# Kernel optimization log

Measured on AMD Instinct MI355X. Metric: run time of the kernel, lower is better.

The kernel has to match this reference:

```python
import jax, jax.numpy as jnp
import numpy as np

EMBED = 1024
HEADS = 16
HEAD_DIM = EMBED // HEADS
SEQ = 2048
BATCH = 2


def setup_inputs() -> dict:
    key = jax.random.key(0)
    ks = jax.random.split(key, 5)
    s = 1.0 / np.sqrt(EMBED)
    return {
        "x": jax.random.normal(ks[0], (BATCH, SEQ, EMBED), jnp.float32),
        "W_qkv": jax.random.uniform(ks[1], (EMBED, 3 * EMBED), jnp.float32, -s, s),
        "b_qkv": jax.random.uniform(ks[2], (3 * EMBED,), jnp.float32, -s, s),
        "W_out": jax.random.uniform(ks[3], (EMBED, EMBED), jnp.float32, -s, s),
        "b_out": jax.random.uniform(ks[4], (EMBED,), jnp.float32, -s, s),
    }


def reference(x, W_qkv, b_qkv, W_out, b_out):
    B, S, E = x.shape
    qkv = x @ W_qkv + b_qkv                      # [B,S,3E]
    q, k, v = jnp.split(qkv, 3, axis=-1)
    # [B,S,E] -> [B,H,S,D]
    def heads(t):
        return t.reshape(B, S, HEADS, HEAD_DIM).transpose(0, 2, 1, 3)
    q, k, v = heads(q), heads(k), heads(v)
    scores = jnp.einsum("bhid,bhjd->bhij", q, k) / np.sqrt(HEAD_DIM)  # [B,H,S,S]
    causal = jnp.tril(jnp.ones((S, S), bool))
    scores = jnp.where(causal[None, None], scores, -jnp.inf)
    probs = jax.nn.softmax(scores, axis=-1)
    out = jnp.einsum("bhij,bhjd->bhid", probs, v)  # [B,H,S,D]
    out = out.transpose(0, 2, 1, 3).reshape(B, S, E)
    return out @ W_out + b_out
```

## Files before the change

kernel.cpp:

```cpp
#include <hip/hip_runtime.h>
#include <hip/hip_bf16.h>
#include <cstdint>
#include <cstddef>


typedef unsigned short u16;
typedef __attribute__((ext_vector_type(8))) short short8;
typedef __attribute__((ext_vector_type(4))) short short4v;
typedef __attribute__((ext_vector_type(4))) float floatx4;

#define MFMA16(a, b, c) __builtin_amdgcn_mfma_f32_16x16x32_bf16((a), (b), (c), 0, 0, 0)

#if __has_builtin(__builtin_amdgcn_mfma_f32_16x16x16_bf16)
#define PV_MFMA(a, b, c) __builtin_amdgcn_mfma_f32_16x16x16_bf16((a), (b), (c), 0, 0, 0)
#elif __has_builtin(__builtin_amdgcn_mfma_f32_16x16x16bf16_1k)
#define PV_MFMA(a, b, c) __builtin_amdgcn_mfma_f32_16x16x16bf16_1k((a), (b), (c), 0, 0, 0)
#else
static __device__ __forceinline__ floatx4 pv_mfma_asm(short4v a, short4v b, floatx4 c) {
    asm volatile("v_mfma_f32_16x16x16_bf16 %0, %1, %2, %0" : "+v"(c) : "v"(a), "v"(b));
    return c;
}
#define PV_MFMA(a, b, c) pv_mfma_asm((a), (b), (c))
#endif

#if __has_builtin(__builtin_amdgcn_exp2f)
#define EXP2(x) __builtin_amdgcn_exp2f(x)
#else
#define EXP2(x) exp2f(x)
#endif

#define QSCALE 0.18033688011f

static __device__ __forceinline__ u16 f2b(float f) {
    union { float f; uint32_t u; } v; v.f = f;
    return (u16)((v.u + 0x7fffu + ((v.u >> 16) & 1u)) >> 16);
}

static __device__ __forceinline__ uint32_t pkbf(float lo, float hi) {
    union { float f; uint32_t u; } a, b; a.f = lo; b.f = hi;
    return __builtin_amdgcn_perm(b.u + 0x8000u, a.u + 0x8000u, 0x07060302u);
}

static __device__ __forceinline__ void async_cp16(const u16* g, u16* lds_wave_base) {
    __builtin_amdgcn_global_load_lds((__attribute__((address_space(1))) void*)g,
                                     (__attribute__((address_space(3))) void*)lds_wave_base,
                                     16, 0, 0);
}


__global__ __launch_bounds__(256) void k_f32_to_bf16(const float* __restrict__ src,
                                                     u16* __restrict__ dst, int n8) {
    int g = blockIdx.x * 256 + threadIdx.x;
    if (g >= n8) return;
    const float4* s = (const float4*)src + (size_t)g * 2;
    float4 f0 = s[0];
    float4 f1 = s[1];
    alignas(16) u16 r[8] = {f2b(f0.x), f2b(f0.y), f2b(f0.z), f2b(f0.w),
                            f2b(f1.x), f2b(f1.y), f2b(f1.z), f2b(f1.w)};
    *(uint4*)(dst + (size_t)g * 8) = *(const uint4*)r;
}

__global__ __launch_bounds__(256) void k_transpose_to_bf16(const float* __restrict__ src,
                                                           u16* __restrict__ dst,
                                                           int R, int C) {
    __shared__ float t[32][33];
    int tx = threadIdx.x, ty = threadIdx.y;
    int c0 = blockIdx.x * 32, r0 = blockIdx.y * 32;
#pragma unroll
    for (int i = 0; i < 4; ++i)
        t[ty + i * 8][tx] = src[(size_t)(r0 + ty + i * 8) * C + c0 + tx];
    __syncthreads();
#pragma unroll
    for (int i = 0; i < 4; ++i)
        dst[(size_t)(c0 + ty + i * 8) * R + r0 + tx] = f2b(t[tx][ty + i * 8]);
}


__global__ __launch_bounds__(256) void k_qkv_gemm(const u16* __restrict__ A,
                                                  const u16* __restrict__ Bt,
                                                  const float* __restrict__ bias,
                                                  u16* __restrict__ Qb,
                                                  u16* __restrict__ Kb,
                                                  u16* __restrict__ Vtb) {
    __shared__ __align__(16) u16 As[128 * 64];
    __shared__ __align__(16) u16 Bs[128 * 64];
    int tid = threadIdx.x;
    int w = tid >> 6, lane = tid & 63, quad = lane >> 4, l16 = lane & 15;
    int wm = w >> 1, wn = w & 1;
    int m0 = blockIdx.y * 128, n0 = blockIdx.x * 128;
    int wb8 = (tid & ~63) * 8;
    floatx4 acc[4][4] = {};

    for (int kt = 0; kt < 16; ++kt) {
#pragma unroll
        for (int i = 0; i < 4; ++i) {
            int f = i * 256 + tid;
            int r = f >> 3, c = (f & 7) ^ (r & 7);
            async_cp16(&A[(size_t)(m0 + r) * 1024 + kt * 64 + c * 8], &As[i * 2048 + wb8]);
        }
#pragma unroll
        for (int i = 0; i < 4; ++i) {
            int f = i * 256 + tid;
            int r = f >> 3, c = (f & 7) ^ (r & 7);
            async_cp16(&Bt[(size_t)(n0 + r) * 1024 + kt * 64 + c * 8], &Bs[i * 2048 + wb8]);
        }
        __syncthreads();
#pragma unroll
        for (int ks = 0; ks < 2; ++ks) {
            short8 af[4], bf[4];
            int sw = l16 & 7;
#pragma unroll
            for (int mt = 0; mt < 4; ++mt)
                af[mt] = *(const short8*)&As[((wm * 64 + mt * 16 + l16) * 8 + ((ks * 4 + quad) ^ sw)) * 8];
#pragma unroll
            for (int nt = 0; nt < 4; ++nt)
                bf[nt] = *(const short8*)&Bs[((wn * 64 + nt * 16 + l16) * 8 + ((ks * 4 + quad) ^ sw)) * 8];
#pragma unroll
            for (int mt = 0; mt < 4; ++mt)
#pragma unroll
                for (int nt = 0; nt < 4; ++nt)
                    acc[mt][nt] = MFMA16(af[mt], bf[nt], acc[mt][nt]);
        }
        __syncthreads();
    }

    int region = n0 >> 10;
    if (region == 2) {
#pragma unroll
        for (int mt = 0; mt < 4; ++mt)
#pragma unroll
            for (int nt = 0; nt < 4; ++nt) {
                int n_abs = n0 + wn * 64 + nt * 16 + l16;
                int e = n_abs & 1023, h = e >> 6, d = e & 63;
                float vb = bias[n_abs];
                int mrow = m0 + wm * 64 + mt * 16 + quad * 4;
                int b = mrow >> 11, s0 = mrow & 2047;
                uint2 val;
                val.x = pkbf(acc[mt][nt][0] + vb, acc[mt][nt][1] + vb);
                val.y = pkbf(acc[mt][nt][2] + vb, acc[mt][nt][3] + vb);
                *(uint2*)&Vtb[((size_t)(b * 16 + h) * 64 + d) * 2048 + s0] = val;
            }
    } else {
        u16* dst = region == 0 ? Qb : Kb;
        float scl = region == 0 ? QSCALE : 1.0f;
#pragma unroll
        for (int mt = 0; mt < 4; ++mt)
#pragma unroll
            for (int nt = 0; nt < 4; ++nt)
#pragma unroll
                for (int r = 0; r < 4; ++r) {
                    int m_abs = m0 + wm * 64 + mt * 16 + quad * 4 + r;
                    int n_abs = n0 + wn * 64 + nt * 16 + l16;
                    float val = (acc[mt][nt][r] + bias[n_abs]) * scl;
                    int e = n_abs & 1023, h = e >> 6, d = e & 63;
                    int b = m_abs >> 11, s = m_abs & 2047;
                    dst[((size_t)(b * 16 + h) * 2048 + s) * 64 + d] = f2b(val);
                }
    }
}


__global__ __launch_bounds__(256) void k_out_gemm(const u16* __restrict__ A,
                                                  const u16* __restrict__ Bt,
                                                  const float* __restrict__ bias,
                                                  float* __restrict__ out) {
    __shared__ __align__(16) u16 As[64 * 64];
    __shared__ __align__(16) u16 Bs[128 * 64];
    int tid = threadIdx.x;
    int w = tid >> 6, lane = tid & 63, quad = lane >> 4, l16 = lane & 15;
    int wm = w >> 1, wn = w & 1;
    int m0 = blockIdx.y * 64, n0 = blockIdx.x * 128;
    int wb8 = (tid & ~63) * 8;
    floatx4 acc[2][4] = {};

    for (int kt = 0; kt < 16; ++kt) {
#pragma unroll
        for (int i = 0; i < 2; ++i) {
            int f = i * 256 + tid;
            int r = f >> 3, c = (f & 7) ^ (r & 7);
            async_cp16(&A[(size_t)(m0 + r) * 1024 + kt * 64 + c * 8], &As[i * 2048 + wb8]);
        }
#pragma unroll
        for (int i = 0; i < 4; ++i) {
            int f = i * 256 + tid;
            int r = f >> 3, c = (f & 7) ^ (r & 7);
            async_cp16(&Bt[(size_t)(n0 + r) * 1024 + kt * 64 + c * 8], &Bs[i * 2048 + wb8]);
        }
        __syncthreads();
#pragma unroll
        for (int ks = 0; ks < 2; ++ks) {
            short8 af[2], bf[4];
            int sw = l16 & 7;
#pragma unroll
            for (int mt = 0; mt < 2; ++mt)
                af[mt] = *(const short8*)&As[((wm * 32 + mt * 16 + l16) * 8 + ((ks * 4 + quad) ^ sw)) * 8];
#pragma unroll
            for (int nt = 0; nt < 4; ++nt)
                bf[nt] = *(const short8*)&Bs[((wn * 64 + nt * 16 + l16) * 8 + ((ks * 4 + quad) ^ sw)) * 8];
#pragma unroll
            for (int mt = 0; mt < 2; ++mt)
#pragma unroll
                for (int nt = 0; nt < 4; ++nt)
                    acc[mt][nt] = MFMA16(af[mt], bf[nt], acc[mt][nt]);
        }
        __syncthreads();
    }

#pragma unroll
    for (int mt = 0; mt < 2; ++mt)
#pragma unroll
        for (int nt = 0; nt < 4; ++nt)
#pragma unroll
            for (int r = 0; r < 4; ++r) {
                int m_abs = m0 + wm * 32 + mt * 16 + quad * 4 + r;
                int n_abs = n0 + wn * 64 + nt * 16 + l16;
                out[(size_t)m_abs * 1024 + n_abs] = acc[mt][nt][r] + bias[n_abs];
            }
}


__global__ __launch_bounds__(256, 2) void k_attn(const u16* __restrict__ Qb,
                                                 const u16* __restrict__ Kb,
                                                 const u16* __restrict__ Vtb,
                                                 u16* __restrict__ attnb) {
    __shared__ __align__(16) u16 KV[4][2][4096];
    int tid = threadIdx.x;
    int w = tid >> 6, lane = tid & 63, quad = lane >> 4, l16 = lane & 15;
    int L = blockIdx.x;
    int bh = ((L & 7) << 2) | ((L >> 3) & 3);
    int pr = L >> 5;
    int qta = pr, qtb = 31 - pr;
    const u16* Qp = Qb + (size_t)bh * 131072;
    const u16* Kp = Kb + (size_t)bh * 131072;
    const u16* Vp = Vtb + (size_t)bh * 131072;

    int r0 = tid >> 3, c0 = ((tid & 7) ^ (r0 & 7)) * 8;
    int f1 = 256 + tid;
    int r1 = f1 >> 3, c1 = ((f1 & 7) ^ (r1 & 7)) * 8;
    int kOff0 = r0 * 64 + c0, kOff1 = r1 * 64 + c1;
    int vOff0 = r0 * 2048 + c0, vOff1 = r1 * 2048 + c1;
    int wb = (tid & ~63) * 8;

    int qrowa = qta * 64 + w * 16 + l16;
    int qrowb = qtb * 64 + w * 16 + l16;
    short8 qa0 = *(const short8*)&Qp[(size_t)qrowa * 64 + quad * 8];
    short8 qa1 = *(const short8*)&Qp[(size_t)qrowa * 64 + 32 + quad * 8];
    short8 qb0 = *(const short8*)&Qp[(size_t)qrowb * 64 + quad * 8];
    short8 qb1 = *(const short8*)&Qp[(size_t)qrowb * 64 + 32 + quad * 8];

    int na = qta + 1;
    int n = na + qtb + 1;

    auto stage = [&](int j) {
        int kt = (j < na) ? j : (j - na);
        u16* Ks = (u16*)KV[j & 3][0];
        u16* Vs = (u16*)KV[j & 3][1];
        const u16* kp = Kp + (size_t)kt * 4096;
        const u16* vp = Vp + (size_t)kt * 64;
        async_cp16(kp + kOff0, Ks + wb);
        async_cp16(kp + kOff1, Ks + 2048 + wb);
        async_cp16(vp + vOff0, Vs + wb);
        async_cp16(vp + vOff1, Vs + 2048 + wb);
    };

    floatx4 accO[4] = {};
    float m_run = -__builtin_inff(), l_run = 0.f;
    int sw = l16 & 7;
    int kt = 0, qt = qta, q0 = qta * 64;
    short8 cq0 = qa0, cq1 = qa1;
    int b = bh >> 4, h = bh & 15;

    stage(0); stage(1); stage(2);

    for (int j = 0; j < n; ++j) {
        asm volatile("s_waitcnt vmcnt(8)" ::: "memory");
        asm volatile("s_barrier" ::: "memory");
        {
            int jn = j + 3;
            stage(jn < n ? jn : n - 1);
        }
        const u16* Ks = (const u16*)KV[j & 3][0];
        const u16* Vs = (const u16*)KV[j & 3][1];

        floatx4 sa[4] = {};
#pragma unroll
        for (int nt = 0; nt < 4; ++nt) {
            int rb = (nt * 16 + l16) * 8;
            short8 kfa = *(const short8*)&Ks[(rb + (quad ^ sw)) * 8];
            short8 kfb = *(const short8*)&Ks[(rb + ((4 + quad) ^ sw)) * 8];
            sa[nt] = MFMA16(kfa, cq0, sa[nt]);
            sa[nt] = MFMA16(kfb, cq1, sa[nt]);
        }
        if (kt == qt) {
            int q_abs = q0 + w * 16 + l16;
#pragma unroll
            for (int nt = 0; nt < 4; ++nt)
#pragma unroll
                for (int r = 0; r < 4; ++r)
                    if (kt * 64 + nt * 16 + quad * 4 + r > q_abs)
                        sa[nt][r] = -__builtin_inff();
        }
        float v = sa[0][0];
#pragma unroll
        for (int nt = 0; nt < 4; ++nt)
#pragma unroll
            for (int r = 0; r < 4; ++r) v = fmaxf(v, sa[nt][r]);
        v = fmaxf(v, __shfl_xor(v, 16));
        v = fmaxf(v, __shfl_xor(v, 32));
        float m_new = fmaxf(m_run, v);
        float alpha = EXP2(m_run - m_new);
        float p[4][4];
        float rs = 0.f;
#pragma unroll
        for (int nt = 0; nt < 4; ++nt)
#pragma unroll
            for (int r = 0; r < 4; ++r) {
                float e = EXP2(sa[nt][r] - m_new);
                p[nt][r] = e;
                rs += e;
            }
        rs += __shfl_xor(rs, 16);
        rs += __shfl_xor(rs, 32);
        l_run = l_run * alpha + rs;
        m_run = m_new;
        float al[4];
#pragma unroll
        for (int r = 0; r < 4; ++r) al[r] = __shfl(alpha, quad * 4 + r, 16);
#pragma unroll
        for (int dt = 0; dt < 4; ++dt)
#pragma unroll
            for (int r = 0; r < 4; ++r) accO[dt][r] *= al[r];
#pragma unroll
        for (int nt = 0; nt < 4; ++nt) {
            union { uint2 u; short4v s; } pf;
            pf.u.x = pkbf(p[nt][0], p[nt][1]);
            pf.u.y = pkbf(p[nt][2], p[nt][3]);
#pragma unroll
            for (int dt = 0; dt < 4; ++dt) {
                int row = dt * 16 + l16;
                int chunk = nt * 2 + (quad >> 1);
                const char* vb2 = (const char*)Vs + row * 128 + ((chunk ^ (row & 7)) * 16) + (quad & 1) * 8;
                short4v vf = *(const short4v*)vb2;
                accO[dt] = PV_MFMA(pf.s, vf, accO[dt]);
            }
        }

        if (kt == qt) {
            float lbc[4];
#pragma unroll
            for (int r = 0; r < 4; ++r) lbc[r] = __shfl(l_run, quad * 4 + r, 16);
#pragma unroll
            for (int r = 0; r < 4; ++r) {
                float inv = 1.f / lbc[r];
                int q_abs = q0 + w * 16 + quad * 4 + r;
                size_t base = ((size_t)(b * 2048 + q_abs)) * 1024 + h * 64;
#pragma unroll
                for (int dt = 0; dt < 4; ++dt)
                    attnb[base + dt * 16 + l16] = f2b(accO[dt][r] * inv);
            }
#pragma unroll
            for (int dt = 0; dt < 4; ++dt) accO[dt] = floatx4{0.f, 0.f, 0.f, 0.f};
            m_run = -__builtin_inff();
            l_run = 0.f;
            kt = 0;
            qt = qtb;
            q0 = qtb * 64;
            cq0 = qb0;
            cq1 = qb1;
        } else {
            ++kt;
        }
    }
}


extern "C" void kernel_launch(void* const* d_in, const int* in_sizes, int n_in,
                              void* d_out, int out_size, void* d_ws, size_t ws_size,
                              hipStream_t stream) {
    const float* x     = (const float*)d_in[0];
    const float* W_qkv = (const float*)d_in[1];
    const float* b_qkv = (const float*)d_in[2];
    const float* W_out = (const float*)d_in[3];
    const float* b_out = (const float*)d_in[4];
    float* out = (float*)d_out;

    char* p = (char*)d_ws;
    u16* xb    = (u16*)p; p += (size_t)4096 * 1024 * 2;
    u16* wqkvT = (u16*)p; p += (size_t)3072 * 1024 * 2;
    u16* woutT = (u16*)p; p += (size_t)1024 * 1024 * 2;
    u16* Qb    = (u16*)p; p += (size_t)32 * 2048 * 64 * 2;
    u16* Kb    = (u16*)p; p += (size_t)32 * 2048 * 64 * 2;
    u16* Vtb   = (u16*)p; p += (size_t)32 * 64 * 2048 * 2;
    u16* attnb = xb;

    k_f32_to_bf16<<<(4096 * 1024 / 8) / 256, 256, 0, stream>>>(x, xb, 4096 * 1024 / 8);
    dim3 tb(32, 8);
    k_transpose_to_bf16<<<dim3(3072 / 32, 1024 / 32), tb, 0, stream>>>(W_qkv, wqkvT, 1024, 3072);
    k_transpose_to_bf16<<<dim3(1024 / 32, 1024 / 32), tb, 0, stream>>>(W_out, woutT, 1024, 1024);
    k_qkv_gemm<<<dim3(24, 32), 256, 0, stream>>>(xb, wqkvT, b_qkv, Qb, Kb, Vtb);
    k_attn<<<512, 256, 0, stream>>>(Qb, Kb, Vtb, attnb);
    k_out_gemm<<<dim3(8, 64), 256, 0, stream>>>(attnb, woutT, b_out, out);
}
```

Baseline: 194.1 us.

## Share K/V tiles between both paired query tiles in causal attention loop

Instead of streaming K/V separately for the short and long query tiles in sequence, the loop now walks only the long tile's key range and applies each loaded K/V tile to both query tiles, computing the short tile only while kt <= qta. This halves K/V staging and LDS fragment reads for the overlapping range. The PV MFMA operands are swapped so the output is transposed, which lets the epilogue write packed bf16 vectors without cross-lane alpha/l broadcasts. Block-to-tile pairing is also remapped to spread heavy and light tiles differently. The cost is higher register pressure from two accumulators and the preloaded V fragments.

```diff
diff --git a/kernel.cpp b/kernel.cpp
--- a/kernel.cpp
+++ b/kernel.cpp
@@ -228,11 +228,13 @@
     int w = tid >> 6, lane = tid & 63, quad = lane >> 4, l16 = lane & 15;
     int L = blockIdx.x;
     int bh = ((L & 7) << 2) | ((L >> 3) & 3);
-    int pr = L >> 5;
+    int idx = (L >> 5) & 15;
+    int pr = idx < 8 ? idx : 23 - idx;
     int qta = pr, qtb = 31 - pr;
     const u16* Qp = Qb + (size_t)bh * 131072;
     const u16* Kp = Kb + (size_t)bh * 131072;
     const u16* Vp = Vtb + (size_t)bh * 131072;
+    int b = bh >> 4, h = bh & 15;
 
     int r0 = tid >> 3, c0 = ((tid & 7) ^ (r0 & 7)) * 8;
     int f1 = 256 + tid;
@@ -248,129 +250,127 @@
     short8 qb0 = *(const short8*)&Qp[(size_t)qrowb * 64 + quad * 8];
     short8 qb1 = *(const short8*)&Qp[(size_t)qrowb * 64 + 32 + quad * 8];
 
-    int na = qta + 1;
-    int n = na + qtb + 1;
+    int n = qtb + 1;
 
     auto stage = [&](int j) {
-        int kt = (j < na) ? j : (j - na);
         u16* Ks = (u16*)KV[j & 3][0];
         u16* Vs = (u16*)KV[j & 3][1];
-        const u16* kp = Kp + (size_t)kt * 4096;
-        const u16* vp = Vp + (size_t)kt * 64;
+        const u16* kp = Kp + (size_t)j * 4096;
+        const u16* vp = Vp + (size_t)j * 64;
         async_cp16(kp + kOff0, Ks + wb);
         async_cp16(kp + kOff1, Ks + 2048 + wb);
         async_cp16(vp + vOff0, Vs + wb);
         async_cp16(vp + vOff1, Vs + 2048 + wb);
     };
 
-    floatx4 accO[4] = {};
-    float m_run = -__builtin_inff(), l_run = 0.f;
+    floatx4 accA[4] = {}, accB[4] = {};
+    float ma = -__builtin_inff(), la = 0.f;
+    float mb = -__builtin_inff(), lb = 0.f;
     int sw = l16 & 7;
-    int kt = 0, qt = qta, q0 = qta * 64;
-    short8 cq0 = qa0, cq1 = qa1;
-    int b = bh >> 4, h = bh & 15;
 
     stage(0); stage(1); stage(2);
 
-    for (int j = 0; j < n; ++j) {
+    for (int kt = 0; kt < n; ++kt) {
         asm volatile("s_waitcnt vmcnt(8)" ::: "memory");
         asm volatile("s_barrier" ::: "memory");
         {
-            int jn = j + 3;
+            int jn = kt + 3;
             stage(jn < n ? jn : n - 1);
         }
-        const u16* Ks = (const u16*)KV[j & 3][0];
-        const u16* Vs = (const u16*)KV[j & 3][1];
-
-        floatx4 sa[4] = {};
+        const u16* Ks = (const u16*)KV[kt & 3][0];
+        const u16* Vs = (const u16*)KV[kt & 3][1];
+
+        short8 kfa[4], kfb[4];
 #pragma unroll
         for (int nt = 0; nt < 4; ++nt) {
             int rb = (nt * 16 + l16) * 8;
-            short8 kfa = *(const short8*)&Ks[(rb + (quad ^ sw)) * 8];
-            short8 kfb = *(const short8*)&Ks[(rb + ((4 + quad) ^ sw)) * 8];
-            sa[nt] = MFMA16(kfa, cq0, sa[nt]);
-            sa[nt] = MFMA16(kfb, cq1, sa[nt]);
-        }
-        if (kt == qt) {
-            int q_abs = q0 + w * 16 + l16;
+            kfa[nt] = *(const short8*)&Ks[(rb + (quad ^ sw)) * 8];
+            kfb[nt] = *(const short8*)&Ks[(rb + ((4 + quad) ^ sw)) * 8];
+        }
+        short4v vf[4][4];
+#pragma unroll
+        for (int dt = 0; dt < 4; ++dt) {
+            const char* rowb = (const char*)Vs + (dt * 16 + l16) * 128 + (quad & 1) * 8;
+#pragma unroll
+            for (int nt = 0; nt < 4; ++nt) {
+                int chunk = nt * 2 + (quad >> 1);
+                vf[nt][dt] = *(const short4v*)(rowb + ((chunk ^ sw) * 16));
+            }
+        }
+
+        auto tile_step = [&](short8 qf0, short8 qf1, int qt_this, float& mr, float& lr,
+                             floatx4* accO) {
+            floatx4 sa[4] = {};
+#pragma unroll
+            for (int nt = 0; nt < 4; ++nt) {
+                sa[nt] = MFMA16(kfa[nt], qf0, sa[nt]);
+                sa[nt] = MFMA16(kfb[nt], qf1, sa[nt]);
+            }
+            if (kt == qt_this) {
+                int q_abs = qt_this * 64 + w * 16 + l16;
+#pragma unroll
+                for (int nt = 0; nt < 4; ++nt)
+#pragma unroll
+                    for (int r = 0; r < 4; ++r)
+                        if (kt * 64 + nt * 16 + quad * 4 + r > q_abs)
+                            sa[nt][r] = -__builtin_inff();
+            }
+            float v = sa[0][0];
 #pragma unroll
             for (int nt = 0; nt < 4; ++nt)
 #pragma unroll
-                for (int r = 0; r < 4; ++r)
-                    if (kt * 64 + nt * 16 + quad * 4 + r > q_abs)
-                        sa[nt][r] = -__builtin_inff();
-        }
-        float v = sa[0][0];
-#pragma unroll
-        for (int nt = 0; nt < 4; ++nt)
-#pragma unroll
-            for (int r = 0; r < 4; ++r) v = fmaxf(v, sa[nt][r]);
-        v = fmaxf(v, __shfl_xor(v, 16));
-        v = fmaxf(v, __shfl_xor(v, 32));
-        float m_new = fmaxf(m_run, v);
-        float alpha = EXP2(m_run - m_new);
-        float p[4][4];
-        float rs = 0.f;
-#pragma unroll
-        for (int nt = 0; nt < 4; ++nt)
-#pragma unroll
-            for (int r = 0; r < 4; ++r) {
-                float e = EXP2(sa[nt][r] - m_new);
-                p[nt][r] = e;
-                rs += e;
-            }
-        rs += __shfl_xor(rs, 16);
-        rs += __shfl_xor(rs, 32);
-        l_run = l_run * alpha + rs;
-        m_run = m_new;
-        float al[4];
-#pragma unroll
-        for (int r = 0; r < 4; ++r) al[r] = __shfl(alpha, quad * 4 + r, 16);
-#pragma unroll
-        for (int dt = 0; dt < 4; ++dt)
-#pragma unroll
-            for (int r = 0; r < 4; ++r) accO[dt][r] *= al[r];
-#pragma unroll
-        for (int nt = 0; nt < 4; ++nt) {
-            union { uint2 u; short4v s; } pf;
-            pf.u.x = pkbf(p[nt][0], p[nt][1]);
-            pf.u.y = pkbf(p[nt][2], p[nt][3]);
-#pragma unroll
-            for (int dt = 0; dt < 4; ++dt) {
-                int row = dt * 16 + l16;
-                int chunk = nt * 2 + (quad >> 1);
-                const char* vb2 = (const char*)Vs + row * 128 + ((chunk ^ (row & 7)) * 16) + (quad & 1) * 8;
-                short4v vf = *(const short4v*)vb2;
-                accO[dt] = PV_MFMA(pf.s, vf, accO[dt]);
-            }
-        }
-
-        if (kt == qt) {
-            float lbc[4];
-#pragma unroll
-            for (int r = 0; r < 4; ++r) lbc[r] = __shfl(l_run, quad * 4 + r, 16);
-#pragma unroll
-            for (int r = 0; r < 4; ++r) {
-                float inv = 1.f / lbc[r];
-                int q_abs = q0 + w * 16 + quad * 4 + r;
-                size_t base = ((size_t)(b * 2048 + q_abs)) * 1024 + h * 64;
+                for (int r = 0; r < 4; ++r) v = fmaxf(v, sa[nt][r]);
+            v = fmaxf(v, __shfl_xor(v, 16));
+            v = fmaxf(v, __shfl_xor(v, 32));
+            float m_new = fmaxf(mr, v);
+            float alpha = EXP2(mr - m_new);
+            float p[4][4];
+            float rs = 0.f;
+#pragma unroll
+            for (int nt = 0; nt < 4; ++nt)
+#pragma unroll
+                for (int r = 0; r < 4; ++r) {
+                    float e = EXP2(sa[nt][r] - m_new);
+                    p[nt][r] = e;
+                    rs += e;
+                }
+            rs += __shfl_xor(rs, 16);
+            rs += __shfl_xor(rs, 32);
+            lr = lr * alpha + rs;
+            mr = m_new;
+#pragma unroll
+            for (int dt = 0; dt < 4; ++dt)
+#pragma unroll
+                for (int r = 0; r < 4; ++r) accO[dt][r] *= alpha;
+#pragma unroll
+            for (int nt = 0; nt < 4; ++nt) {
+                union { uint2 u; short4v s; } pf;
+                pf.u.x = pkbf(p[nt][0], p[nt][1]);
+                pf.u.y = pkbf(p[nt][2], p[nt][3]);
 #pragma unroll
                 for (int dt = 0; dt < 4; ++dt)
-                    attnb[base + dt * 16 + l16] = f2b(accO[dt][r] * inv);
-            }
-#pragma unroll
-            for (int dt = 0; dt < 4; ++dt) accO[dt] = floatx4{0.f, 0.f, 0.f, 0.f};
-            m_run = -__builtin_inff();
-            l_run = 0.f;
-            kt = 0;
-            qt = qtb;
-            q0 = qtb * 64;
-            cq0 = qb0;
-            cq1 = qb1;
-        } else {
-            ++kt;
-        }
+                    accO[dt] = PV_MFMA(vf[nt][dt], pf.s, accO[dt]);
+            }
+        };
+
+        tile_step(qb0, qb1, qtb, mb, lb, accB);
+        if (kt <= qta) tile_step(qa0, qa1, qta, ma, la, accA);
     }
+
+    auto epilogue = [&](int qt_this, float lr, const floatx4* accO) {
+        int q_abs = qt_this * 64 + w * 16 + l16;
+        float inv = 1.f / lr;
+        size_t base = ((size_t)(b * 2048 + q_abs)) * 1024 + h * 64;
+#pragma unroll
+        for (int dt = 0; dt < 4; ++dt) {
+            uint2 val;
+            val.x = pkbf(accO[dt][0] * inv, accO[dt][1] * inv);
+            val.y = pkbf(accO[dt][2] * inv, accO[dt][3] * inv);
+            *(uint2*)&attnb[base + dt * 16 + quad * 4] = val;
+        }
+    };
+    epilogue(qta, la, accA);
+    epilogue(qtb, lb, accB);
 }
 
 
```

Result: faster. 189.8 us (-2.2%).
